# Kernel tuning notes

Measured on AMD Instinct MI355X. Metric: run time of the kernel, lower is better.

## Reference

```python
import jax, jax.numpy as jnp
import numpy as np

H, W = 256, 256  # hardcoded data_shape in the original module
MEAN_MODULO = 0.25


def _conv_valid(x, k):
    # x: [h, w], k: [kh, kw]; torch F.conv2d is cross-correlation, as is lax conv
    return jax.lax.conv_general_dilated(
        x[None, None], k[None, None], window_strides=(1, 1), padding='VALID'
    )[0, 0]


def _forward(pred_E, pred_v, data):
    f32 = jnp.float32
    # --- strain from displacement (is_strain=False path) ---
    kx = jnp.array([[-0.5, -0.5], [0.5, 0.5]], f32)   # strain_conv_x weight
    ky = jnp.array([[0.5, -0.5], [0.5, -0.5]], f32)   # strain_conv_y weight
    ux = data[:, 0].reshape(H + 1, W + 1)
    uy = data[:, 1].reshape(H + 1, W + 1)
    e_xx = 100.0 * _conv_valid(ux, kx)                 # [256,256]
    e_yy = 100.0 * _conv_valid(uy, ky)
    r_xy = 100.0 * (_conv_valid(ux, ky) + _conv_valid(uy, kx))

    # --- stress: per-pixel 3x3 plane-stress matrix, expressed elementwise ---
    E = pred_E.reshape(H, W)
    v = pred_v.reshape(H, W)
    frac = E / (1.0 - v * v)
    s_xx = (e_xx + v * e_yy) * frac
    s_yy = (v * e_xx + e_yy) * frac
    s_xy = r_xy * (1.0 - v) * 0.5 * frac

    # --- residual (equilibrium) losses ---
    sum_k = jnp.ones((3, 3), f32)
    wx_xx = jnp.array([[-1., -1., -1.], [0., 0., 0.], [1., 1., 1.]], f32)
    wx_xy = jnp.array([[1., 0., -1.], [1., 0., -1.], [1., 0., -1.]], f32)
    wy_yy = wx_xy  # same kernel values in the source
    wy_xy = wx_xx

    E_conv = _conv_valid(E, sum_k)                     # [254,254]
    fx = _conv_valid(s_xx, wx_xx) + _conv_valid(s_xy, wx_xy)
    fy = _conv_valid(s_yy, wy_yy) + _conv_valid(s_xy, wy_xy)
    loss_x = jnp.mean(jnp.abs(fx / E_conv))
    loss_y = jnp.mean(jnp.abs(fy / E_conv))

    loss_e = jnp.abs(jnp.mean(E) - MEAN_MODULO)
    return loss_x + loss_y + loss_e / 100.0


def setup_inputs() -> dict:
    key = jax.random.key(0)
    k1, k2, k3 = jax.random.split(key, 3)
    pred_E = jax.random.uniform(k1, (H * W,), jnp.float32, 0.05, 0.5)
    pred_v = jax.random.uniform(k2, (H * W,), jnp.float32, 0.05, 0.45)
    data = 0.01 * jax.random.normal(k3, ((H + 1) * (W + 1), 2), jnp.float32)
    return {"pred_E": pred_E, "pred_v": pred_v, "data": data}


def reference(pred_E, pred_v, data):
    return _forward(pred_E, pred_v, data)
```

## Files before the change

### kernel.cpp

```cpp
#include <hip/hip_runtime.h>


#define HH 256
#define WW 256
#define DPITCH 257
#define NBLK 256
#define TAG_MAGIC 0x5BD1E995u

struct S3 { float xx, yy, xy; };

__device__ __forceinline__ S3 stress_at(const float2* __restrict__ d2,
                                        const float* __restrict__ E,
                                        const float* __restrict__ V,
                                        int r, int c) {
    const int base = r * DPITCH + c;
    const float2 p00 = d2[base];
    const float2 p01 = d2[base + 1];
    const float2 p10 = d2[base + DPITCH];
    const float2 p11 = d2[base + DPITCH + 1];
    const float exx = 50.f * ((p10.x + p11.x) - (p00.x + p01.x));
    const float eyy = 50.f * ((p00.y - p01.y) + (p10.y - p11.y));
    const float rxy = 50.f * ((p00.x - p01.x) + (p10.x - p11.x))
                    + 50.f * ((p10.y + p11.y) - (p00.y + p01.y));
    const int idx = r * WW + c;
    const float Ev = E[idx];
    const float vv = V[idx];
    const float frac = Ev / (1.f - vv * vv);
    S3 s;
    s.xx = (exx + vv * eyy) * frac;
    s.yy = (vv * exx + eyy) * frac;
    s.xy = rxy * (1.f - vv) * 0.5f * frac;
    return s;
}

__global__ __launch_bounds__(256) void inverse_loss_onepass(
        const float* __restrict__ E, const float* __restrict__ V,
        const float* __restrict__ data, float* __restrict__ ws,
        float* __restrict__ out) {
    const int t = blockIdx.x * 256 + threadIdx.x;
    const int r = t >> 8;
    const int c = t & 255;
    const float2* d2 = (const float2*)data;

    float sE = E[t];
    float ax = 0.f, ay = 0.f;

    if (r < HH - 2 && c < WW - 2) {
        float ec = 0.f;
        #pragma unroll
        for (int a = 0; a < 3; ++a) {
            #pragma unroll
            for (int b = 0; b < 3; ++b) ec += E[(r + a) * WW + (c + b)];
        }
        const S3 s00 = stress_at(d2, E, V, r,     c);
        const S3 s01 = stress_at(d2, E, V, r,     c + 1);
        const S3 s02 = stress_at(d2, E, V, r,     c + 2);
        const S3 s10 = stress_at(d2, E, V, r + 1, c);
        const S3 s12 = stress_at(d2, E, V, r + 1, c + 2);
        const S3 s20 = stress_at(d2, E, V, r + 2, c);
        const S3 s21 = stress_at(d2, E, V, r + 2, c + 1);
        const S3 s22 = stress_at(d2, E, V, r + 2, c + 2);
        const float fx = (s20.xx + s21.xx + s22.xx) - (s00.xx + s01.xx + s02.xx)
                       + (s00.xy + s10.xy + s20.xy) - (s02.xy + s12.xy + s22.xy);
        const float fy = (s00.yy + s10.yy + s20.yy) - (s02.yy + s12.yy + s22.yy)
                       + (s20.xy + s21.xy + s22.xy) - (s00.xy + s01.xy + s02.xy);
        ax = fabsf(fx / ec);
        ay = fabsf(fy / ec);
    }

    #pragma unroll
    for (int off = 32; off > 0; off >>= 1) {
        ax += __shfl_down(ax, off);
        ay += __shfl_down(ay, off);
        sE += __shfl_down(sE, off);
    }
    __shared__ float red[3][4];
    const int wave = threadIdx.x >> 6;
    const int lane = threadIdx.x & 63;
    if (lane == 0) { red[0][wave] = ax; red[1][wave] = ay; red[2][wave] = sE; }
    __syncthreads();

    if (threadIdx.x == 0) {
        const float p0 = red[0][0] + red[0][1] + red[0][2] + red[0][3];
        const float p1 = red[1][0] + red[1][1] + red[1][2] + red[1][3];
        const float p2 = red[2][0] + red[2][1] + red[2][2] + red[2][3];
        const int b = blockIdx.x;
        __hip_atomic_store(&ws[b],            p0, __ATOMIC_RELAXED, __HIP_MEMORY_SCOPE_AGENT);
        __hip_atomic_store(&ws[NBLK + b],     p1, __ATOMIC_RELAXED, __HIP_MEMORY_SCOPE_AGENT);
        __hip_atomic_store(&ws[2 * NBLK + b], p2, __ATOMIC_RELAXED, __HIP_MEMORY_SCOPE_AGENT);
        const unsigned tag = __float_as_uint(p0) ^ __float_as_uint(p1)
                           ^ __float_as_uint(p2) ^ TAG_MAGIC;
        __hip_atomic_store((unsigned*)&ws[3 * NBLK + b], tag,
                           __ATOMIC_RELEASE, __HIP_MEMORY_SCOPE_AGENT);
    }

    if (blockIdx.x == 0) {
        const int i = threadIdx.x;
        float v0, v1, v2;
        unsigned tag;
        do {
            tag = __hip_atomic_load((const unsigned*)&ws[3 * NBLK + i],
                                    __ATOMIC_ACQUIRE, __HIP_MEMORY_SCOPE_AGENT);
            v0 = __hip_atomic_load(&ws[i],            __ATOMIC_RELAXED, __HIP_MEMORY_SCOPE_AGENT);
            v1 = __hip_atomic_load(&ws[NBLK + i],     __ATOMIC_RELAXED, __HIP_MEMORY_SCOPE_AGENT);
            v2 = __hip_atomic_load(&ws[2 * NBLK + i], __ATOMIC_RELAXED, __HIP_MEMORY_SCOPE_AGENT);
        } while (tag != (__float_as_uint(v0) ^ __float_as_uint(v1)
                         ^ __float_as_uint(v2) ^ TAG_MAGIC));

        #pragma unroll
        for (int off = 32; off > 0; off >>= 1) {
            v0 += __shfl_down(v0, off);
            v1 += __shfl_down(v1, off);
            v2 += __shfl_down(v2, off);
        }
        __shared__ float red2[3][4];
        if (lane == 0) { red2[0][wave] = v0; red2[1][wave] = v1; red2[2][wave] = v2; }
        __syncthreads();
        if (threadIdx.x == 0) {
            const float gx = red2[0][0] + red2[0][1] + red2[0][2] + red2[0][3];
            const float gy = red2[1][0] + red2[1][1] + red2[1][2] + red2[1][3];
            const float gE = red2[2][0] + red2[2][1] + red2[2][2] + red2[2][3];
            const float npix = (float)((HH - 2) * (WW - 2));
            out[0] = gx / npix + gy / npix
                   + fabsf(gE * (1.f / (HH * WW)) - 0.25f) * 0.01f;
        }
    }
}

extern "C" void kernel_launch(void* const* d_in, const int* in_sizes, int n_in,
                              void* d_out, int out_size, void* d_ws, size_t ws_size,
                              hipStream_t stream) {
    const float* E    = (const float*)d_in[0];
    const float* V    = (const float*)d_in[1];
    const float* data = (const float*)d_in[2];
    float* out = (float*)d_out;
    float* ws  = (float*)d_ws;
    inverse_loss_onepass<<<dim3(NBLK), dim3(256), 0, stream>>>(E, V, data, ws, out);
}
```

Before: 10.90 us.

## Share per-row stress values via LDS and use last-block counter for final reduction

Each block now handles one output row. Every thread computes stress for three rows at its own column and stores them in shared memory, so the 3x3 stencil reads from LDS. Before, each thread recomputed eight stress values from global memory. The spin-wait on per-block tags in block 0 is replaced by an atomic ticket counter, and the last block to finish does the final reduction. The counter is never reset but is taken modulo NBLK, so it relies on the workspace persisting consistently across calls.

```diff
diff --git a/kernel.cpp b/kernel.cpp
--- a/kernel.cpp
+++ b/kernel.cpp
@@ -5,65 +5,59 @@
 #define WW 256
 #define DPITCH 257
 #define NBLK 256
-#define TAG_MAGIC 0x5BD1E995u
-
-struct S3 { float xx, yy, xy; };
-
-__device__ __forceinline__ S3 stress_at(const float2* __restrict__ d2,
-                                        const float* __restrict__ E,
-                                        const float* __restrict__ V,
-                                        int r, int c) {
-    const int base = r * DPITCH + c;
-    const float2 p00 = d2[base];
-    const float2 p01 = d2[base + 1];
-    const float2 p10 = d2[base + DPITCH];
-    const float2 p11 = d2[base + DPITCH + 1];
-    const float exx = 50.f * ((p10.x + p11.x) - (p00.x + p01.x));
-    const float eyy = 50.f * ((p00.y - p01.y) + (p10.y - p11.y));
-    const float rxy = 50.f * ((p00.x - p01.x) + (p10.x - p11.x))
-                    + 50.f * ((p10.y + p11.y) - (p00.y + p01.y));
-    const int idx = r * WW + c;
-    const float Ev = E[idx];
-    const float vv = V[idx];
-    const float frac = Ev / (1.f - vv * vv);
-    S3 s;
-    s.xx = (exx + vv * eyy) * frac;
-    s.yy = (vv * exx + eyy) * frac;
-    s.xy = rxy * (1.f - vv) * 0.5f * frac;
-    return s;
-}
 
 __global__ __launch_bounds__(256) void inverse_loss_onepass(
         const float* __restrict__ E, const float* __restrict__ V,
         const float* __restrict__ data, float* __restrict__ ws,
         float* __restrict__ out) {
-    const int t = blockIdx.x * 256 + threadIdx.x;
-    const int r = t >> 8;
-    const int c = t & 255;
+    const int r = blockIdx.x;
+    const int c = threadIdx.x;
     const float2* d2 = (const float2*)data;
 
-    float sE = E[t];
+    __shared__ float sxx[3][WW], syy[3][WW], sxy[3][WW], ecol[WW];
+
+    float sE = E[r * WW + c];
     float ax = 0.f, ay = 0.f;
 
+    if (r < HH - 2) {
+        float2 P[4], Q[4];
+        #pragma unroll
+        for (int m = 0; m < 4; ++m) {
+            P[m] = d2[(r + m) * DPITCH + c];
+            Q[m] = d2[(r + m) * DPITCH + c + 1];
+        }
+        float ecs = 0.f;
+        #pragma unroll
+        for (int k = 0; k < 3; ++k) {
+            const float2 p00 = P[k],     p01 = Q[k];
+            const float2 p10 = P[k + 1], p11 = Q[k + 1];
+            const float exx = 50.f * ((p10.x + p11.x) - (p00.x + p01.x));
+            const float eyy = 50.f * ((p00.y - p01.y) + (p10.y - p11.y));
+            const float rxy = 50.f * ((p00.x - p01.x) + (p10.x - p11.x))
+                            + 50.f * ((p10.y + p11.y) - (p00.y + p01.y));
+            const int idx = (r + k) * WW + c;
+            const float Ev = (k == 0) ? sE : E[idx];
+            const float vv = V[idx];
+            const float frac = Ev / (1.f - vv * vv);
+            sxx[k][c] = (exx + vv * eyy) * frac;
+            syy[k][c] = (vv * exx + eyy) * frac;
+            sxy[k][c] = rxy * (1.f - vv) * 0.5f * frac;
+            ecs += Ev;
+        }
+        ecol[c] = ecs;
+    }
+    __syncthreads();
+
     if (r < HH - 2 && c < WW - 2) {
-        float ec = 0.f;
-        #pragma unroll
-        for (int a = 0; a < 3; ++a) {
-            #pragma unroll
-            for (int b = 0; b < 3; ++b) ec += E[(r + a) * WW + (c + b)];
-        }
-        const S3 s00 = stress_at(d2, E, V, r,     c);
-        const S3 s01 = stress_at(d2, E, V, r,     c + 1);
-        const S3 s02 = stress_at(d2, E, V, r,     c + 2);
-        const S3 s10 = stress_at(d2, E, V, r + 1, c);
-        const S3 s12 = stress_at(d2, E, V, r + 1, c + 2);
-        const S3 s20 = stress_at(d2, E, V, r + 2, c);
-        const S3 s21 = stress_at(d2, E, V, r + 2, c + 1);
-        const S3 s22 = stress_at(d2, E, V, r + 2, c + 2);
-        const float fx = (s20.xx + s21.xx + s22.xx) - (s00.xx + s01.xx + s02.xx)
-                       + (s00.xy + s10.xy + s20.xy) - (s02.xy + s12.xy + s22.xy);
-        const float fy = (s00.yy + s10.yy + s20.yy) - (s02.yy + s12.yy + s22.yy)
-                       + (s20.xy + s21.xy + s22.xy) - (s00.xy + s01.xy + s02.xy);
+        const float ec = ecol[c] + ecol[c + 1] + ecol[c + 2];
+        const float fx = (sxx[2][c] + sxx[2][c+1] + sxx[2][c+2])
+                       - (sxx[0][c] + sxx[0][c+1] + sxx[0][c+2])
+                       + (sxy[0][c] + sxy[1][c] + sxy[2][c])
+                       - (sxy[0][c+2] + sxy[1][c+2] + sxy[2][c+2]);
+        const float fy = (syy[0][c] + syy[1][c] + syy[2][c])
+                       - (syy[0][c+2] + syy[1][c+2] + syy[2][c+2])
+                       + (sxy[2][c] + sxy[2][c+1] + sxy[2][c+2])
+                       - (sxy[0][c] + sxy[0][c+1] + sxy[0][c+2]);
         ax = fabsf(fx / ec);
         ay = fabsf(fy / ec);
     }
@@ -75,6 +69,7 @@
         sE += __shfl_down(sE, off);
     }
     __shared__ float red[3][4];
+    __shared__ int is_last;
     const int wave = threadIdx.x >> 6;
     const int lane = threadIdx.x & 63;
     if (lane == 0) { red[0][wave] = ax; red[1][wave] = ay; red[2][wave] = sE; }
@@ -88,25 +83,17 @@
         __hip_atomic_store(&ws[b],            p0, __ATOMIC_RELAXED, __HIP_MEMORY_SCOPE_AGENT);
         __hip_atomic_store(&ws[NBLK + b],     p1, __ATOMIC_RELAXED, __HIP_MEMORY_SCOPE_AGENT);
         __hip_atomic_store(&ws[2 * NBLK + b], p2, __ATOMIC_RELAXED, __HIP_MEMORY_SCOPE_AGENT);
-        const unsigned tag = __float_as_uint(p0) ^ __float_as_uint(p1)
-                           ^ __float_as_uint(p2) ^ TAG_MAGIC;
-        __hip_atomic_store((unsigned*)&ws[3 * NBLK + b], tag,
-                           __ATOMIC_RELEASE, __HIP_MEMORY_SCOPE_AGENT);
+        const unsigned old = __hip_atomic_fetch_add(
+            (unsigned*)&ws[3 * NBLK], 1u, __ATOMIC_ACQ_REL, __HIP_MEMORY_SCOPE_AGENT);
+        is_last = ((old & (NBLK - 1)) == (NBLK - 1)) ? 1 : 0;
     }
+    __syncthreads();
 
-    if (blockIdx.x == 0) {
+    if (is_last) {
         const int i = threadIdx.x;
-        float v0, v1, v2;
-        unsigned tag;
-        do {
-            tag = __hip_atomic_load((const unsigned*)&ws[3 * NBLK + i],
-                                    __ATOMIC_ACQUIRE, __HIP_MEMORY_SCOPE_AGENT);
-            v0 = __hip_atomic_load(&ws[i],            __ATOMIC_RELAXED, __HIP_MEMORY_SCOPE_AGENT);
-            v1 = __hip_atomic_load(&ws[NBLK + i],     __ATOMIC_RELAXED, __HIP_MEMORY_SCOPE_AGENT);
-            v2 = __hip_atomic_load(&ws[2 * NBLK + i], __ATOMIC_RELAXED, __HIP_MEMORY_SCOPE_AGENT);
-        } while (tag != (__float_as_uint(v0) ^ __float_as_uint(v1)
-                         ^ __float_as_uint(v2) ^ TAG_MAGIC));
-
+        float v0 = __hip_atomic_load(&ws[i],            __ATOMIC_RELAXED, __HIP_MEMORY_SCOPE_AGENT);
+        float v1 = __hip_atomic_load(&ws[NBLK + i],     __ATOMIC_RELAXED, __HIP_MEMORY_SCOPE_AGENT);
+        float v2 = __hip_atomic_load(&ws[2 * NBLK + i], __ATOMIC_RELAXED, __HIP_MEMORY_SCOPE_AGENT);
         #pragma unroll
         for (int off = 32; off > 0; off >>= 1) {
             v0 += __shfl_down(v0, off);
```

New measurement: 14.07 us. 29.1% more time.
